# Performance work log

Hardware: AMD Instinct MI355X
Metric: run time of the kernel (lower is better)

## Reference

```python
import jax, jax.numpy as jnp
import numpy as np

B, T, V, E, U = 64, 512, 32000, 1024, 1024


def setup_inputs() -> dict:
    key = jax.random.key(0)
    k0, k1, k2, k3 = jax.random.split(key, 4)
    x = jax.random.randint(k0, (B, T), 0, V, dtype=jnp.int32)
    hidden = jnp.zeros((B, U), jnp.float32)
    emb = jax.random.normal(k1, (V, E), jnp.float32) * 0.02
    Wx = jax.random.normal(k2, (E, 3 * U), jnp.float32) / np.sqrt(E).astype(np.float32)
    Wh = jax.random.normal(k3, (U, 3 * U), jnp.float32) / np.sqrt(U).astype(np.float32)
    b_i = jnp.zeros((3 * U,), jnp.float32)  # input bias (reset_after=True has 2 biases)
    b_r = jnp.zeros((3 * U,), jnp.float32)  # recurrent bias
    return {"x": x, "hidden": hidden, "emb": emb, "Wx": Wx, "Wh": Wh, "b_i": b_i, "b_r": b_r}


def reference(x, hidden, emb, Wx, Wh, b_i, b_r):
    # Embedding with mask_zero=True: mask = (token != 0)
    mask = (x != 0)                                   # [B,T]
    e = jnp.take(emb, x, axis=0)                      # [B,T,E]
    # Precompute all input projections in one big GEMM (z|r|h gate order, Keras layout)
    xp = jnp.einsum('bte,eu->btu', e, Wx) + b_i       # [B,T,3U]
    xp_t = jnp.moveaxis(xp, 1, 0)                     # [T,B,3U] time-major for scan
    m_t = jnp.moveaxis(mask, 1, 0)[..., None]         # [T,B,1]

    def step(h, inp):
        xpt, m = inp
        hp = h @ Wh + b_r                             # [B,3U]
        xz, xr, xh = jnp.split(xpt, 3, axis=-1)
        hz, hr, hh = jnp.split(hp, 3, axis=-1)
        z = jax.nn.sigmoid(xz + hz)
        r = jax.nn.sigmoid(xr + hr)
        cand = jnp.tanh(xh + r * hh)                  # reset_after=True: r applied post-matmul
        h_new = z * h + (1.0 - z) * cand
        h_new = jnp.where(m, h_new, h)                # masked steps copy state through
        return h_new, h_new

    state, out_t = jax.lax.scan(step, hidden, (xp_t, m_t))
    output = jnp.moveaxis(out_t, 0, 1)                # [B,T,U]
    return output, state
```

## Files before the change

kernel.cpp:

```cpp
#include <hip/hip_runtime.h>
#include <stdint.h>


#define B_SZ   64
#define T_LEN  512
#define U_DIM  1024
#define E_DIM  1024
#define G3     3072
#define BU     (B_SZ * U_DIM)
#define XP_SCALE 131072.0f
#define XP_INV   (1.0f / 131072.0f)
#define LDT    40
#define NWG    256
#define GRPWG  64

typedef unsigned short ushort_t;
typedef __attribute__((ext_vector_type(8))) short bf16x8;
typedef __attribute__((ext_vector_type(4))) float f32x4;

__device__ __forceinline__ ushort_t f2bf(float f) {
  unsigned u = __builtin_bit_cast(unsigned, f);
  u += 0x7fffu + ((u >> 16) & 1u);
  return (ushort_t)(u >> 16);
}
__device__ __forceinline__ float bf2f(ushort_t h) {
  return __builtin_bit_cast(float, (unsigned)h << 16);
}

__device__ __forceinline__ bf16x8 ldg_cohere_b128(const ushort_t* p) {
  bf16x8 r;
  asm volatile("global_load_dwordx4 %0, %1, off sc0 sc1"
               : "=v"(r) : "v"(p) : "memory");
  return r;
}
__device__ __forceinline__ void stg_cohere_u16(ushort_t* p, unsigned v) {
  asm volatile("global_store_short %0, %1, off sc0 sc1"
               :: "v"(p), "v"(v) : "memory");
}
__device__ __forceinline__ unsigned ldg_cohere_u32(const unsigned* p) {
  unsigned r;
  asm volatile("global_load_dword %0, %1, off sc0 sc1\n\ts_waitcnt vmcnt(0)"
               : "=v"(r) : "v"(p) : "memory");
  return r;
}
__device__ __forceinline__ int ldg_sshort(const short* p) {
  int r;
  asm volatile("global_load_sshort %0, %1, off"
               : "=v"(r) : "v"(p) : "memory");
  return r;
}
__device__ __forceinline__ int ldg_s32(const int* p) {
  int r;
  asm volatile("global_load_dword %0, %1, off"
               : "=v"(r) : "v"(p) : "memory");
  return r;
}
#define WAITV(n) do { asm volatile("s_waitcnt vmcnt(" #n ")" ::: "memory"); \
                      __builtin_amdgcn_sched_barrier(0); } while (0)

__global__ __launch_bounds__(256) void gemm_xp(
    const float* __restrict__ emb,
    const float* __restrict__ Wx,
    const int* __restrict__ x,
    const float* __restrict__ b_i,
    short* __restrict__ xp)
{
  __shared__ ushort_t aH[128 * LDT];
  __shared__ ushort_t aL[128 * LDT];
  __shared__ ushort_t bH[128 * LDT];
  __shared__ ushort_t bL[128 * LDT];
  const int tid = threadIdx.x, lane = tid & 63, w = tid >> 6;
  const int bx = blockIdx.x;
  const int nIdx = bx % 24, mIdx = bx / 24;
  const int m0 = mIdx * 128, n0 = nIdx * 128;

  const int aRow0 = tid >> 2, aRow1 = (tid + 256) >> 2, aKoct = tid & 3;
  const size_t aBase0 = (size_t)x[m0 + aRow0] * E_DIM + (size_t)aKoct * 8;
  const size_t aBase1 = (size_t)x[m0 + aRow1] * E_DIM + (size_t)aKoct * 8;
  const int bN = tid & 127, bKoct0 = tid >> 7;

  const int wr = (w >> 1) * 64, wc = (w & 1) * 64;
  f32x4 acc[4][4];
#pragma unroll
  for (int i = 0; i < 4; i++)
#pragma unroll
    for (int j = 0; j < 4; j++) acc[i][j] = (f32x4){0.f, 0.f, 0.f, 0.f};

  for (int k0 = 0; k0 < E_DIM; k0 += 32) {
    __syncthreads();
#pragma unroll
    for (int pp = 0; pp < 2; ++pp) {
      const float* src = emb + (pp ? aBase1 : aBase0) + k0;
      int row = pp ? aRow1 : aRow0;
      float4 v0 = *(const float4*)(src);
      float4 v1 = *(const float4*)(src + 4);
      float vv[8] = {v0.x, v0.y, v0.z, v0.w, v1.x, v1.y, v1.z, v1.w};
      bf16x8 oh, ol;
#pragma unroll
      for (int j = 0; j < 8; ++j) {
        ushort_t hi = f2bf(vv[j]);
        oh[j] = (short)hi;
        ol[j] = (short)f2bf(vv[j] - bf2f(hi));
      }
      int off = row * LDT + aKoct * 8;
      *(bf16x8*)&aH[off] = oh;
      *(bf16x8*)&aL[off] = ol;
    }
#pragma unroll
    for (int kk = 0; kk < 2; ++kk) {
      int koct = bKoct0 + 2 * kk;
      float vv[8];
#pragma unroll
      for (int e = 0; e < 8; ++e)
        vv[e] = Wx[(size_t)(k0 + koct * 8 + e) * G3 + n0 + bN];
      bf16x8 oh, ol;
#pragma unroll
      for (int j = 0; j < 8; ++j) {
        ushort_t hi = f2bf(vv[j]);
        oh[j] = (short)hi;
        ol[j] = (short)f2bf(vv[j] - bf2f(hi));
      }
      int off = bN * LDT + koct * 8;
      *(bf16x8*)&bH[off] = oh;
      *(bf16x8*)&bL[off] = ol;
    }
    __syncthreads();
    bf16x8 afH[4], afL[4], bfH[4], bfL[4];
#pragma unroll
    for (int mi = 0; mi < 4; mi++) {
      int off = (wr + mi * 16 + (lane & 15)) * LDT + (lane >> 4) * 8;
      afH[mi] = *(const bf16x8*)&aH[off];
      afL[mi] = *(const bf16x8*)&aL[off];
    }
#pragma unroll
    for (int ni = 0; ni < 4; ni++) {
      int off = (wc + ni * 16 + (lane & 15)) * LDT + (lane >> 4) * 8;
      bfH[ni] = *(const bf16x8*)&bH[off];
      bfL[ni] = *(const bf16x8*)&bL[off];
    }
#pragma unroll
    for (int mi = 0; mi < 4; mi++)
#pragma unroll
      for (int ni = 0; ni < 4; ni++) {
        acc[mi][ni] = __builtin_amdgcn_mfma_f32_16x16x32_bf16(afH[mi], bfH[ni], acc[mi][ni], 0, 0, 0);
        acc[mi][ni] = __builtin_amdgcn_mfma_f32_16x16x32_bf16(afH[mi], bfL[ni], acc[mi][ni], 0, 0, 0);
        acc[mi][ni] = __builtin_amdgcn_mfma_f32_16x16x32_bf16(afL[mi], bfH[ni], acc[mi][ni], 0, 0, 0);
      }
  }
#pragma unroll
  for (int ni = 0; ni < 4; ni++) {
    int col = n0 + wc + ni * 16 + (lane & 15);
    float bias = b_i[col];
#pragma unroll
    for (int mi = 0; mi < 4; mi++) {
      int rbase = m0 + wr + mi * 16 + (lane >> 4) * 4;
#pragma unroll
      for (int i = 0; i < 4; i++) {
        int m = rbase + i;
        int b = m >> 9, t = m & 511;
        float v = acc[mi][ni][i] + bias;
        int q = __float2int_rn(v * XP_SCALE);
        q = q > 32767 ? 32767 : (q < -32768 ? -32768 : q);
        xp[(size_t)(t * 64 + b) * G3 + col] = (short)q;
      }
    }
  }
}

__global__ __launch_bounds__(256) void init_h(
    const float* __restrict__ hidden,
    ushort_t* __restrict__ hHI, ushort_t* __restrict__ hLO,
    unsigned* __restrict__ cnt)
{
  const int i = blockIdx.x * 256 + threadIdx.x;
  if (blockIdx.x == 0 && threadIdx.x < 256) cnt[threadIdx.x] = 0u;
  if (i < BU) {
    const float v = hidden[i];
    const ushort_t hi = f2bf(v);
    hHI[i] = hi;
    hLO[i] = f2bf(v - bf2f(hi));
  }
}

__global__ __launch_bounds__(512) void gru_scan(
    const float* __restrict__ hidden,
    const float* __restrict__ Wh,
    const float* __restrict__ b_r,
    const short* __restrict__ xp,
    const int* __restrict__ x,
    ushort_t* __restrict__ hHI,
    ushort_t* __restrict__ hLO,
    unsigned* __restrict__ cnt,
    float* __restrict__ out)
{
  __shared__ float part[8][3][64][4];
  const int tid  = threadIdx.x;
  const int lane = tid & 63;
  const int w    = tid >> 6;
  const int bx   = (int)blockIdx.x;
  const int uj   = bx & 63, bi = bx >> 6;
  const int u0   = uj * 16, b0 = bi * 16;
  const int c16  = lane & 15;
  const int kg   = lane >> 4;
  unsigned* mycnt = cnt + bi * 64;

  bf16x8 BH[4][3], BL[4][3];
#pragma unroll
  for (int ks = 0; ks < 4; ++ks)
#pragma unroll
    for (int g = 0; g < 3; ++g) {
      bf16x8 bh, bl;
#pragma unroll
      for (int j = 0; j < 8; ++j) {
        int k = w * 128 + ks * 32 + kg * 8 + j;
        float v = Wh[(size_t)k * G3 + g * 1024 + u0 + c16];
        ushort_t hi = f2bf(v);
        bh[j] = (short)hi;
        bl[j] = (short)f2bf(v - bf2f(hi));
      }
      BH[ks][g] = bh;
      BL[ks][g] = bl;
    }

  const bool epi = (tid < 256);
  const int ebl = (tid >> 4) & 15, eul = tid & 15;
  const int eb = b0 + ebl, eu = u0 + eul;
  float brz = 0.f, brr = 0.f, brh = 0.f, hp = 0.f;
  if (epi) {
    brz = b_r[eu]; brr = b_r[1024 + eu]; brh = b_r[2048 + eu];
    hp  = hidden[(size_t)eb * U_DIM + eu];
  }

  asm volatile("s_waitcnt vmcnt(0) lgkmcnt(0)" ::: "memory");

  int xq0 = 0, xq1 = 0, xq2 = 0, xtok = 0;
  if (epi) {
    xq0 = ldg_sshort(xp + (size_t)eb * G3 + eu);
    xq1 = ldg_sshort(xp + (size_t)eb * G3 + 1024 + eu);
    xq2 = ldg_sshort(xp + (size_t)eb * G3 + 2048 + eu);
    xtok = ldg_s32(x + eb * T_LEN + 0);
  }

  unsigned target = 0;
  unsigned spins = 0;
  for (int t = 0; t < T_LEN; ++t) {
    const ushort_t* __restrict__ rH = hHI + (size_t)(t & 1) * BU;
    const ushort_t* __restrict__ rL = hLO + (size_t)(t & 1) * BU;
    ushort_t* __restrict__ wrH = hHI + (size_t)((t + 1) & 1) * BU;
    ushort_t* __restrict__ wrL = hLO + (size_t)((t + 1) & 1) * BU;

    const ushort_t* pH = rH + (size_t)(b0 + c16) * U_DIM + w * 128 + kg * 8;
    const ushort_t* pL = rL + (size_t)(b0 + c16) * U_DIM + w * 128 + kg * 8;

    f32x4 acc[3];
#pragma unroll
    for (int g = 0; g < 3; ++g) acc[g] = (f32x4){0.f, 0.f, 0.f, 0.f};

    bf16x8 AH0, AL0, AH1, AL1, AH2, AL2, AH3, AL3;
    AH0 = ldg_cohere_b128(pH + 0 * 32);  AL0 = ldg_cohere_b128(pL + 0 * 32);
    AH1 = ldg_cohere_b128(pH + 1 * 32);  AL1 = ldg_cohere_b128(pL + 1 * 32);
    AH2 = ldg_cohere_b128(pH + 2 * 32);  AL2 = ldg_cohere_b128(pL + 2 * 32);
    AH3 = ldg_cohere_b128(pH + 3 * 32);  AL3 = ldg_cohere_b128(pL + 3 * 32);

#define COMP(AH_, AL_, ks_) \
    _Pragma("unroll") \
    for (int g = 0; g < 3; ++g) { \
      acc[g] = __builtin_amdgcn_mfma_f32_16x16x32_bf16(AH_, BH[ks_][g], acc[g], 0, 0, 0); \
      acc[g] = __builtin_amdgcn_mfma_f32_16x16x32_bf16(AH_, BL[ks_][g], acc[g], 0, 0, 0); \
      acc[g] = __builtin_amdgcn_mfma_f32_16x16x32_bf16(AL_, BH[ks_][g], acc[g], 0, 0, 0); \
    }
    WAITV(6);
    COMP(AH0, AL0, 0)
    WAITV(4);
    COMP(AH1, AL1, 1)
    WAITV(2);
    COMP(AH2, AL2, 2)
    WAITV(0);
    COMP(AH3, AL3, 3)
#undef COMP

#pragma unroll
    for (int g = 0; g < 3; ++g)
      *(f32x4*)&part[w][g][lane][0] = acc[g];

    __syncthreads();

    if (epi) {
      const int pl = (ebl >> 2) * 16 + eul, pe = ebl & 3;
      float sz = 0.f, sr = 0.f, sh = 0.f;
#pragma unroll
      for (int s = 0; s < 8; ++s) {
        sz += part[s][0][pl][pe];
        sr += part[s][1][pl][pe];
        sh += part[s][2][pl][pe];
      }

      const float hz = sz + brz, hr = sr + brr, hhv = sh + brh;
      const float xz = (float)xq0 * XP_INV;
      const float xr = (float)xq1 * XP_INV;
      const float xh = (float)xq2 * XP_INV;
      const float z = 1.f / (1.f + __expf(-(xz + hz)));
      const float r = 1.f / (1.f + __expf(-(xr + hr)));
      const float ca = xh + r * hhv;
      const float cand = 1.f - 2.f / (__expf(2.f * ca) + 1.f);
      float hn = z * hp + (1.f - z) * cand;
      hn = (xtok != 0) ? hn : hp;
      hp = hn;

      out[((size_t)eb * T_LEN + t) * U_DIM + eu] = hn;
      const ushort_t hi = f2bf(hn);
      const ushort_t lo = f2bf(hn - bf2f(hi));
      stg_cohere_u16(wrH + (size_t)eb * U_DIM + eu, (unsigned)hi);
      stg_cohere_u16(wrL + (size_t)eb * U_DIM + eu, (unsigned)lo);

      const int tp = (t < T_LEN - 1) ? t + 1 : t;
      xq0 = ldg_sshort(xp + ((size_t)tp * B_SZ + eb) * G3 + eu);
      xq1 = ldg_sshort(xp + ((size_t)tp * B_SZ + eb) * G3 + 1024 + eu);
      xq2 = ldg_sshort(xp + ((size_t)tp * B_SZ + eb) * G3 + 2048 + eu);
      xtok = ldg_s32(x + eb * T_LEN + tp);
      WAITV(4);
    }

    target += GRPWG;
    __syncthreads();
    if (tid == 0)
      __hip_atomic_fetch_add(mycnt, 1u, __ATOMIC_RELAXED, __HIP_MEMORY_SCOPE_AGENT);
    if (w == 0) {
      while (spins < (1u << 22)) {
        if (ldg_cohere_u32(mycnt) >= target) break;
        __builtin_amdgcn_s_sleep(2);
        ++spins;
      }
    }
    __syncthreads();
    __builtin_amdgcn_sched_barrier(0);
  }

  if (epi)
    out[(size_t)B_SZ * T_LEN * U_DIM + (size_t)eb * U_DIM + eu] = hp;
}

extern "C" void kernel_launch(void* const* d_in, const int* in_sizes, int n_in,
                              void* d_out, int out_size, void* d_ws, size_t ws_size,
                              hipStream_t stream) {
  const int*   x      = (const int*)  d_in[0];
  const float* hidden = (const float*)d_in[1];
  const float* emb    = (const float*)d_in[2];
  const float* Wx     = (const float*)d_in[3];
  const float* Wh     = (const float*)d_in[4];
  const float* b_i    = (const float*)d_in[5];
  const float* b_r    = (const float*)d_in[6];
  float* out = (float*)d_out;

  const size_t XP_B = (size_t)T_LEN * B_SZ * G3 * 2;
  const size_t NEED = XP_B + 8 * (size_t)BU + 1024;
  if (ws_size < NEED) return;

  short*    xp  = (short*)d_ws;
  ushort_t* hHI = (ushort_t*)((char*)d_ws + XP_B);
  ushort_t* hLO = hHI + 2 * (size_t)BU;
  unsigned* cnt = (unsigned*)(hLO + 2 * (size_t)BU);

  init_h<<<BU / 256, 256, 0, stream>>>(hidden, hHI, hLO, cnt);
  gemm_xp<<<(32768 / 128) * (G3 / 128), 256, 0, stream>>>(emb, Wx, x, b_i, xp);
  gru_scan<<<NWG, 512, 0, stream>>>(hidden, Wh, b_r, xp, x, hHI, hLO, cnt, out);
}
```

Measured before the change: 3.082 ms.

## Replace atomic counter barrier with per-wave flags polled by one wave

The per-step inter-workgroup barrier changes from a shared atomic counter to per-wave flag words. Each epilogue wave writes its step number with a coherent store right after its own h stores complete, so the workgroup-wide __syncthreads before signalling goes away. A single wave polls all 256 group flags with vector loads, no sleep, and a ballot. The global output store also moves later so it overlaps the coherent h writes. This aims to cut barrier latency across the 512 sequential steps, at the cost of more polling traffic and a tighter spin cap.

```diff
diff --git a/kernel.cpp b/kernel.cpp
--- a/kernel.cpp
+++ b/kernel.cpp
@@ -17,6 +17,7 @@
 typedef unsigned short ushort_t;
 typedef __attribute__((ext_vector_type(8))) short bf16x8;
 typedef __attribute__((ext_vector_type(4))) float f32x4;
+typedef __attribute__((ext_vector_type(4))) unsigned int u32x4;
 
 __device__ __forceinline__ ushort_t f2bf(float f) {
   unsigned u = __builtin_bit_cast(unsigned, f);
@@ -37,9 +38,13 @@
   asm volatile("global_store_short %0, %1, off sc0 sc1"
                :: "v"(p), "v"(v) : "memory");
 }
-__device__ __forceinline__ unsigned ldg_cohere_u32(const unsigned* p) {
-  unsigned r;
-  asm volatile("global_load_dword %0, %1, off sc0 sc1\n\ts_waitcnt vmcnt(0)"
+__device__ __forceinline__ void stg_cohere_u32(unsigned* p, unsigned v) {
+  asm volatile("global_store_dword %0, %1, off sc0 sc1"
+               :: "v"(p), "v"(v) : "memory");
+}
+__device__ __forceinline__ u32x4 ldg_cohere_u32x4(const unsigned* p) {
+  u32x4 r;
+  asm volatile("global_load_dwordx4 %0, %1, off sc0 sc1\n\ts_waitcnt vmcnt(0)"
                : "=v"(r) : "v"(p) : "memory");
   return r;
 }
@@ -170,10 +175,10 @@
 __global__ __launch_bounds__(256) void init_h(
     const float* __restrict__ hidden,
     ushort_t* __restrict__ hHI, ushort_t* __restrict__ hLO,
-    unsigned* __restrict__ cnt)
+    unsigned* __restrict__ flags)
 {
   const int i = blockIdx.x * 256 + threadIdx.x;
-  if (blockIdx.x == 0 && threadIdx.x < 256) cnt[threadIdx.x] = 0u;
+  if (blockIdx.x < 4) flags[blockIdx.x * 256 + threadIdx.x] = 0u;
   if (i < BU) {
     const float v = hidden[i];
     const ushort_t hi = f2bf(v);
@@ -190,7 +195,7 @@
     const int* __restrict__ x,
     ushort_t* __restrict__ hHI,
     ushort_t* __restrict__ hLO,
-    unsigned* __restrict__ cnt,
+    unsigned* __restrict__ flags,
     float* __restrict__ out)
 {
   __shared__ float part[8][3][64][4];
@@ -202,7 +207,7 @@
   const int u0   = uj * 16, b0 = bi * 16;
   const int c16  = lane & 15;
   const int kg   = lane >> 4;
-  unsigned* mycnt = cnt + bi * 64;
+  unsigned* gflags = flags + bi * 256;
 
   bf16x8 BH[4][3], BL[4][3];
 #pragma unroll
@@ -241,7 +246,6 @@
     xtok = ldg_s32(x + eb * T_LEN + 0);
   }
 
-  unsigned target = 0;
   unsigned spins = 0;
   for (int t = 0; t < T_LEN; ++t) {
     const ushort_t* __restrict__ rH = hHI + (size_t)(t & 1) * BU;
@@ -307,7 +311,6 @@
       hn = (xtok != 0) ? hn : hp;
       hp = hn;
 
-      out[((size_t)eb * T_LEN + t) * U_DIM + eu] = hn;
       const ushort_t hi = f2bf(hn);
       const ushort_t lo = f2bf(hn - bf2f(hi));
       stg_cohere_u16(wrH + (size_t)eb * U_DIM + eu, (unsigned)hi);
@@ -318,17 +321,22 @@
       xq1 = ldg_sshort(xp + ((size_t)tp * B_SZ + eb) * G3 + 1024 + eu);
       xq2 = ldg_sshort(xp + ((size_t)tp * B_SZ + eb) * G3 + 2048 + eu);
       xtok = ldg_s32(x + eb * T_LEN + tp);
-      WAITV(4);
-    }
-
-    target += GRPWG;
-    __syncthreads();
-    if (tid == 0)
-      __hip_atomic_fetch_add(mycnt, 1u, __ATOMIC_RELAXED, __HIP_MEMORY_SCOPE_AGENT);
-    if (w == 0) {
-      while (spins < (1u << 22)) {
-        if (ldg_cohere_u32(mycnt) >= target) break;
-        __builtin_amdgcn_s_sleep(2);
+      out[((size_t)eb * T_LEN + t) * U_DIM + eu] = hn;
+      WAITV(5);
+
+      if (lane == 0)
+        stg_cohere_u32(gflags + uj * 4 + w, (unsigned)(t + 1));
+    }
+
+    if (w == 7) {
+      const unsigned* fp = gflags + lane * 4;
+      const unsigned tgt = (unsigned)(t + 1);
+      while (spins < (1u << 18)) {
+        u32x4 f = ldg_cohere_u32x4(fp);
+        unsigned m01 = f[0] < f[1] ? f[0] : f[1];
+        unsigned m23 = f[2] < f[3] ? f[2] : f[3];
+        unsigned mn  = m01 < m23 ? m01 : m23;
+        if (__ballot(mn >= tgt) == ~0ull) break;
         ++spins;
       }
     }
@@ -353,15 +361,15 @@
   float* out = (float*)d_out;
 
   const size_t XP_B = (size_t)T_LEN * B_SZ * G3 * 2;
-  const size_t NEED = XP_B + 8 * (size_t)BU + 1024;
+  const size_t NEED = XP_B + 8 * (size_t)BU + 4096;
   if (ws_size < NEED) return;
 
-  short*    xp  = (short*)d_ws;
-  ushort_t* hHI = (ushort_t*)((char*)d_ws + XP_B);
-  ushort_t* hLO = hHI + 2 * (size_t)BU;
-  unsigned* cnt = (unsigned*)(hLO + 2 * (size_t)BU);
-
-  init_h<<<BU / 256, 256, 0, stream>>>(hidden, hHI, hLO, cnt);
+  short*    xp    = (short*)d_ws;
+  ushort_t* hHI   = (ushort_t*)((char*)d_ws + XP_B);
+  ushort_t* hLO   = hHI + 2 * (size_t)BU;
+  unsigned* flags = (unsigned*)(hLO + 2 * (size_t)BU);
+
+  init_h<<<BU / 256, 256, 0, stream>>>(hidden, hHI, hLO, flags);
   gemm_xp<<<(32768 / 128) * (G3 / 128), 256, 0, stream>>>(emb, Wx, x, b_i, xp);
-  gru_scan<<<NWG, 512, 0, stream>>>(hidden, Wh, b_r, xp, x, hHI, hLO, cnt, out);
-}
+  gru_scan<<<NWG, 512, 0, stream>>>(hidden, Wh, b_r, xp, x, hHI, hLO, flags, out);
+}
```

Result: slower. 4.042 ms (+31.2%).

## Split each batch group into two 8-row halves with independent barrier counters

Applied to the files above, without the earlier changes.

Each workgroup's 16 batch rows are now processed as two sub-chunks of 8 rows, each synchronized by its own grid-wide counter. While one half waits for its step-t hidden state, the other half can proceed, pipelining the barrier latency across the two chunks. MFMA tiles stay 16 rows wide, so half the rows are duplicated and matrix work per step doubles. Barrier count per step also doubles, and the out store now goes through inline asm.

```diff
diff --git a/kernel.cpp b/kernel.cpp
--- a/kernel.cpp
+++ b/kernel.cpp
@@ -27,7 +27,7 @@
   return __builtin_bit_cast(float, (unsigned)h << 16);
 }
 
-__device__ __forceinline__ bf16x8 ldg_cohere_b128(const ushort_t* p) {
+__device__ __forceinline__ bf16x8 ldg_cohere_b128(const void* p) {
   bf16x8 r;
   asm volatile("global_load_dwordx4 %0, %1, off sc0 sc1"
                : "=v"(r) : "v"(p) : "memory");
@@ -54,6 +54,10 @@
   asm volatile("global_load_dword %0, %1, off"
                : "=v"(r) : "v"(p) : "memory");
   return r;
+}
+__device__ __forceinline__ void stg_u32(float* p, float v) {
+  asm volatile("global_store_dword %0, %1, off"
+               :: "v"(p), "v"(v) : "memory");
 }
 #define WAITV(n) do { asm volatile("s_waitcnt vmcnt(" #n ")" ::: "memory"); \
                       __builtin_amdgcn_sched_barrier(0); } while (0)
@@ -173,7 +177,7 @@
     unsigned* __restrict__ cnt)
 {
   const int i = blockIdx.x * 256 + threadIdx.x;
-  if (blockIdx.x == 0 && threadIdx.x < 256) cnt[threadIdx.x] = 0u;
+  if (blockIdx.x < 2) cnt[blockIdx.x * 256 + threadIdx.x] = 0u;
   if (i < BU) {
     const float v = hidden[i];
     const ushort_t hi = f2bf(v);
@@ -198,11 +202,10 @@
   const int lane = tid & 63;
   const int w    = tid >> 6;
   const int bx   = (int)blockIdx.x;
-  const int uj   = bx & 63, bi = bx >> 6;
-  const int u0   = uj * 16, b0 = bi * 16;
+  const int uj   = bx & 63, sgrp = bx >> 6;
+  const int u0   = uj * 16, b0 = sgrp * 16;
   const int c16  = lane & 15;
   const int kg   = lane >> 4;
-  unsigned* mycnt = cnt + bi * 64;
 
   bf16x8 BH[4][3], BL[4][3];
 #pragma unroll
@@ -222,122 +225,140 @@
       BL[ks][g] = bl;
     }
 
-  const bool epi = (tid < 256);
-  const int ebl = (tid >> 4) & 15, eul = tid & 15;
-  const int eb = b0 + ebl, eu = u0 + eul;
-  float brz = 0.f, brr = 0.f, brh = 0.f, hp = 0.f;
+  const bool epi = (tid < 128);
+  const int ebl = tid >> 4, eul = tid & 15;
+  const int eu = u0 + eul;
+  float brz = 0.f, brr = 0.f, brh = 0.f;
+  float hp[2] = {0.f, 0.f};
   if (epi) {
     brz = b_r[eu]; brr = b_r[1024 + eu]; brh = b_r[2048 + eu];
-    hp  = hidden[(size_t)eb * U_DIM + eu];
+    hp[0] = hidden[(size_t)(b0 + ebl) * U_DIM + eu];
+    hp[1] = hidden[(size_t)(b0 + 8 + ebl) * U_DIM + eu];
   }
 
   asm volatile("s_waitcnt vmcnt(0) lgkmcnt(0)" ::: "memory");
 
-  int xq0 = 0, xq1 = 0, xq2 = 0, xtok = 0;
+  int xq[2][3], xtok[2];
+  xq[0][0] = xq[0][1] = xq[0][2] = xq[1][0] = xq[1][1] = xq[1][2] = 0;
+  xtok[0] = xtok[1] = 0;
   if (epi) {
-    xq0 = ldg_sshort(xp + (size_t)eb * G3 + eu);
-    xq1 = ldg_sshort(xp + (size_t)eb * G3 + 1024 + eu);
-    xq2 = ldg_sshort(xp + (size_t)eb * G3 + 2048 + eu);
-    xtok = ldg_s32(x + eb * T_LEN + 0);
-  }
-
-  unsigned target = 0;
+#pragma unroll
+    for (int c = 0; c < 2; ++c) {
+      const int eb = b0 + c * 8 + ebl;
+      xq[c][0] = ldg_sshort(xp + (size_t)eb * G3 + eu);
+      xq[c][1] = ldg_sshort(xp + (size_t)eb * G3 + 1024 + eu);
+      xq[c][2] = ldg_sshort(xp + (size_t)eb * G3 + 2048 + eu);
+      xtok[c]  = ldg_s32(x + eb * T_LEN + 0);
+    }
+  }
+
   unsigned spins = 0;
   for (int t = 0; t < T_LEN; ++t) {
     const ushort_t* __restrict__ rH = hHI + (size_t)(t & 1) * BU;
     const ushort_t* __restrict__ rL = hLO + (size_t)(t & 1) * BU;
     ushort_t* __restrict__ wrH = hHI + (size_t)((t + 1) & 1) * BU;
     ushort_t* __restrict__ wrL = hLO + (size_t)((t + 1) & 1) * BU;
-
-    const ushort_t* pH = rH + (size_t)(b0 + c16) * U_DIM + w * 128 + kg * 8;
-    const ushort_t* pL = rL + (size_t)(b0 + c16) * U_DIM + w * 128 + kg * 8;
-
-    f32x4 acc[3];
-#pragma unroll
-    for (int g = 0; g < 3; ++g) acc[g] = (f32x4){0.f, 0.f, 0.f, 0.f};
-
-    bf16x8 AH0, AL0, AH1, AL1, AH2, AL2, AH3, AL3;
-    AH0 = ldg_cohere_b128(pH + 0 * 32);  AL0 = ldg_cohere_b128(pL + 0 * 32);
-    AH1 = ldg_cohere_b128(pH + 1 * 32);  AL1 = ldg_cohere_b128(pL + 1 * 32);
-    AH2 = ldg_cohere_b128(pH + 2 * 32);  AL2 = ldg_cohere_b128(pL + 2 * 32);
-    AH3 = ldg_cohere_b128(pH + 3 * 32);  AL3 = ldg_cohere_b128(pL + 3 * 32);
+    const unsigned tgt = (unsigned)t * GRPWG;
+
+#pragma unroll
+    for (int c = 0; c < 2; ++c) {
+      const int b0c = b0 + c * 8;
+      unsigned* mycnt = cnt + (2 * sgrp + c) * 64;
+
+      if (w == 0) {
+        while (spins < (1u << 22)) {
+          if (ldg_cohere_u32(mycnt) >= tgt) break;
+          __builtin_amdgcn_s_sleep(2);
+          ++spins;
+        }
+      }
+      __syncthreads();
+
+      const ushort_t* pH = rH + (size_t)(b0c + (c16 & 7)) * U_DIM + w * 128 + kg * 8;
+      const ushort_t* pL = rL + (size_t)(b0c + (c16 & 7)) * U_DIM + w * 128 + kg * 8;
+
+      f32x4 acc[3];
+#pragma unroll
+      for (int g = 0; g < 3; ++g) acc[g] = (f32x4){0.f, 0.f, 0.f, 0.f};
+
+      bf16x8 AH0, AL0, AH1, AL1, AH2, AL2, AH3, AL3;
+      AH0 = ldg_cohere_b128(pH + 0 * 32);  AL0 = ldg_cohere_b128(pL + 0 * 32);
+      AH1 = ldg_cohere_b128(pH + 1 * 32);  AL1 = ldg_cohere_b128(pL + 1 * 32);
+      AH2 = ldg_cohere_b128(pH + 2 * 32);  AL2 = ldg_cohere_b128(pL + 2 * 32);
+      AH3 = ldg_cohere_b128(pH + 3 * 32);  AL3 = ldg_cohere_b128(pL + 3 * 32);
 
 #define COMP(AH_, AL_, ks_) \
-    _Pragma("unroll") \
-    for (int g = 0; g < 3; ++g) { \
-      acc[g] = __builtin_amdgcn_mfma_f32_16x16x32_bf16(AH_, BH[ks_][g], acc[g], 0, 0, 0); \
-      acc[g] = __builtin_amdgcn_mfma_f32_16x16x32_bf16(AH_, BL[ks_][g], acc[g], 0, 0, 0); \
-      acc[g] = __builtin_amdgcn_mfma_f32_16x16x32_bf16(AL_, BH[ks_][g], acc[g], 0, 0, 0); \
-    }
-    WAITV(6);
-    COMP(AH0, AL0, 0)
-    WAITV(4);
-    COMP(AH1, AL1, 1)
-    WAITV(2);
-    COMP(AH2, AL2, 2)
-    WAITV(0);
-    COMP(AH3, AL3, 3)
+      _Pragma("unroll") \
+      for (int g = 0; g < 3; ++g) { \
+        acc[g] = __builtin_amdgcn_mfma_f32_16x16x32_bf16(AH_, BH[ks_][g], acc[g], 0, 0, 0); \
+        acc[g] = __builtin_amdgcn_mfma_f32_16x16x32_bf16(AH_, BL[ks_][g], acc[g], 0, 0, 0); \
+        acc[g] = __builtin_amdgcn_mfma_f32_16x16x32_bf16(AL_, BH[ks_][g], acc[g], 0, 0, 0); \
+      }
+      WAITV(6);
+      COMP(AH0, AL0, 0)
+      WAITV(4);
+      COMP(AH1, AL1, 1)
+      WAITV(2);
+      COMP(AH2, AL2, 2)
+      WAITV(0);
+      COMP(AH3, AL3, 3)
 #undef COMP
 
 #pragma unroll
-    for (int g = 0; g < 3; ++g)
-      *(f32x4*)&part[w][g][lane][0] = acc[g];
-
-    __syncthreads();
-
-    if (epi) {
-      const int pl = (ebl >> 2) * 16 + eul, pe = ebl & 3;
-      float sz = 0.f, sr = 0.f, sh = 0.f;
-#pragma unroll
-      for (int s = 0; s < 8; ++s) {
-        sz += part[s][0][pl][pe];
-        sr += part[s][1][pl][pe];
-        sh += part[s][2][pl][pe];
-      }
-
-      const float hz = sz + brz, hr = sr + brr, hhv = sh + brh;
-      const float xz = (float)xq0 * XP_INV;
-      const float xr = (float)xq1 * XP_INV;
-      const float xh = (float)xq2 * XP_INV;
-      const float z = 1.f / (1.f + __expf(-(xz + hz)));
-      const float r = 1.f / (1.f + __expf(-(xr + hr)));
-      const float ca = xh + r * hhv;
-      const float cand = 1.f - 2.f / (__expf(2.f * ca) + 1.f);
-      float hn = z * hp + (1.f - z) * cand;
-      hn = (xtok != 0) ? hn : hp;
-      hp = hn;
-
-      out[((size_t)eb * T_LEN + t) * U_DIM + eu] = hn;
-      const ushort_t hi = f2bf(hn);
-      const ushort_t lo = f2bf(hn - bf2f(hi));
-      stg_cohere_u16(wrH + (size_t)eb * U_DIM + eu, (unsigned)hi);
-      stg_cohere_u16(wrL + (size_t)eb * U_DIM + eu, (unsigned)lo);
-
-      const int tp = (t < T_LEN - 1) ? t + 1 : t;
-      xq0 = ldg_sshort(xp + ((size_t)tp * B_SZ + eb) * G3 + eu);
-      xq1 = ldg_sshort(xp + ((size_t)tp * B_SZ + eb) * G3 + 1024 + eu);
-      xq2 = ldg_sshort(xp + ((size_t)tp * B_SZ + eb) * G3 + 2048 + eu);
-      xtok = ldg_s32(x + eb * T_LEN + tp);
-      WAITV(4);
-    }
-
-    target += GRPWG;
-    __syncthreads();
-    if (tid == 0)
-      __hip_atomic_fetch_add(mycnt, 1u, __ATOMIC_RELAXED, __HIP_MEMORY_SCOPE_AGENT);
-    if (w == 0) {
-      while (spins < (1u << 22)) {
-        if (ldg_cohere_u32(mycnt) >= target) break;
-        __builtin_amdgcn_s_sleep(2);
-        ++spins;
-      }
-    }
-    __syncthreads();
-    __builtin_amdgcn_sched_barrier(0);
-  }
-
-  if (epi)
-    out[(size_t)B_SZ * T_LEN * U_DIM + (size_t)eb * U_DIM + eu] = hp;
+      for (int g = 0; g < 3; ++g)
+        *(f32x4*)&part[w][g][lane][0] = acc[g];
+
+      __syncthreads();
+
+      if (epi) {
+        const int pl = (ebl >> 2) * 16 + eul, pe = ebl & 3;
+        float sz = 0.f, sr = 0.f, sh = 0.f;
+#pragma unroll
+        for (int ss = 0; ss < 8; ++ss) {
+          sz += part[ss][0][pl][pe];
+          sr += part[ss][1][pl][pe];
+          sh += part[ss][2][pl][pe];
+        }
+
+        const float hz = sz + brz, hr = sr + brr, hhv = sh + brh;
+        const float xz = (float)xq[c][0] * XP_INV;
+        const float xr = (float)xq[c][1] * XP_INV;
+        const float xh = (float)xq[c][2] * XP_INV;
+        const float z = 1.f / (1.f + __expf(-(xz + hz)));
+        const float r = 1.f / (1.f + __expf(-(xr + hr)));
+        const float ca = xh + r * hhv;
+        const float cand = 1.f - 2.f / (__expf(2.f * ca) + 1.f);
+        float hn = z * hp[c] + (1.f - z) * cand;
+        hn = (xtok[c] != 0) ? hn : hp[c];
+        hp[c] = hn;
+
+        const int eb = b0c + ebl;
+        stg_u32(&out[((size_t)eb * T_LEN + t) * U_DIM + eu], hn);
+        const ushort_t hi = f2bf(hn);
+        const ushort_t lo = f2bf(hn - bf2f(hi));
+        stg_cohere_u16(wrH + (size_t)eb * U_DIM + eu, (unsigned)hi);
+        stg_cohere_u16(wrL + (size_t)eb * U_DIM + eu, (unsigned)lo);
+
+        const int tp = (t < T_LEN - 1) ? t + 1 : t;
+        xq[c][0] = ldg_sshort(xp + ((size_t)tp * B_SZ + eb) * G3 + eu);
+        xq[c][1] = ldg_sshort(xp + ((size_t)tp * B_SZ + eb) * G3 + 1024 + eu);
+        xq[c][2] = ldg_sshort(xp + ((size_t)tp * B_SZ + eb) * G3 + 2048 + eu);
+        xtok[c]  = ldg_s32(x + eb * T_LEN + tp);
+        WAITV(4);
+      }
+
+      __syncthreads();
+      if (tid == 0)
+        __hip_atomic_fetch_add(mycnt, 1u, __ATOMIC_RELAXED, __HIP_MEMORY_SCOPE_AGENT);
+      __builtin_amdgcn_sched_barrier(0);
+    }
+  }
+
+  if (epi) {
+#pragma unroll
+    for (int c = 0; c < 2; ++c)
+      out[(size_t)B_SZ * T_LEN * U_DIM + (size_t)(b0 + c * 8 + ebl) * U_DIM + eu] = hp[c];
+  }
 }
 
 extern "C" void kernel_launch(void* const* d_in, const int* in_sizes, int n_in,
@@ -353,7 +374,7 @@
   float* out = (float*)d_out;
 
   const size_t XP_B = (size_t)T_LEN * B_SZ * G3 * 2;
-  const size_t NEED = XP_B + 8 * (size_t)BU + 1024;
+  const size_t NEED = XP_B + 8 * (size_t)BU + 2048;
   if (ws_size < NEED) return;
 
   short*    xp  = (short*)d_ws;
```

Measured after the change: 4.286 ms. +39.1%, slower.
